# Performance work log

Hardware: AMD Instinct MI355X
Metric: run time of the kernel (lower is better)

## Reference

```python
import jax, jax.numpy as jnp
import numpy as np

BT, NQ, NC, C, H, HID = 192, 64, 1024, 384, 8, 1536
DH = C // H                       # 48
SCALE = DH ** -0.5
MAX_NEG = -float(np.finfo(np.float32).max)


def _ln(x, eps, g=None, b=None):
    m = x.mean(-1, keepdims=True)
    v = ((x - m) ** 2).mean(-1, keepdims=True)
    y = (x - m) / jnp.sqrt(v + eps)
    if g is not None:
        y = y * g + b
    return y


def _gelu_tanh(x):
    # GELU(approximate='tanh')
    return 0.5 * x * (1.0 + jnp.tanh(jnp.sqrt(2.0 / jnp.pi) * (x + 0.044715 * x ** 3)))


def setup_inputs() -> dict:
    key = jax.random.key(0)
    ks = jax.random.split(key, 10)
    s = lambda fan: 1.0 / np.sqrt(fan)
    return {
        "x": jax.random.normal(ks[0], (BT, NQ, C), jnp.float32),
        "context": jax.random.normal(ks[1], (BT, NC, C), jnp.float32),
        "mask": jax.random.randint(ks[2], (BT, NQ), 0, 2) > 0,
        "Wq": jax.random.normal(ks[3], (C, C), jnp.float32) * s(C),
        "bq": jnp.zeros((C,), jnp.float32),
        "Wkv": jax.random.normal(ks[4], (C, 2 * C), jnp.float32) * s(C),
        "bkv": jnp.zeros((2 * C,), jnp.float32),
        "Wo": jax.random.normal(ks[5], (C, C), jnp.float32) * s(C),
        "bo": jnp.zeros((C,), jnp.float32),
        "g_ctx": jnp.ones((C,), jnp.float32),
        "b_ctx": jnp.zeros((C,), jnp.float32),
        "W1": jax.random.normal(ks[6], (C, HID), jnp.float32) * s(C),
        "b1": jnp.zeros((HID,), jnp.float32),
        "W2": jax.random.normal(ks[7], (HID, C), jnp.float32) * s(HID),
        "b2": jnp.zeros((C,), jnp.float32),
    }


def reference(x, context, mask, Wq, bq, Wkv, bkv, Wo, bo, g_ctx, b_ctx, W1, b1, W2, b2):
    # --- cross-attention branch ---
    xn = _ln(x, 1e-6)                       # norm1 (no affine)
    cn = _ln(context, 1e-5, g_ctx, b_ctx)   # norm_context (affine, default eps)
    q = (xn @ Wq + bq).reshape(BT, NQ, H, DH).transpose(0, 2, 1, 3)    # (B,H,NQ,DH)
    kv = cn @ Wkv + bkv
    k, v = jnp.split(kv, 2, axis=-1)
    k = k.reshape(BT, NC, H, DH).transpose(0, 2, 1, 3)                 # (B,H,NC,DH)
    v = v.reshape(BT, NC, H, DH).transpose(0, 2, 1, 3)
    sim = jnp.einsum('bhqd,bhkd->bhqk', q, k) * SCALE                  # (B,H,NQ,NC)
    # mask shape (BT, NQ): True = keep query row; ~mask * (-max) bias
    bias = jnp.where(mask[:, None, :, None], 0.0, MAX_NEG)
    attn = jax.nn.softmax(sim + bias, axis=-1)
    o = jnp.einsum('bhqk,bhkd->bhqd', attn, v).transpose(0, 2, 1, 3).reshape(BT, NQ, C)
    x = x + o @ Wo + bo
    # --- MLP branch ---
    xn2 = _ln(x, 1e-6)                      # norm2 (no affine)
    x = x + _gelu_tanh(xn2 @ W1 + b1) @ W2 + b2
    return x
```

## Files before the change

kernel.cpp:

```cpp
#include <hip/hip_runtime.h>
#include <hip/hip_bf16.h>
#include <math.h>

typedef unsigned int  u32;
typedef unsigned short u16;
typedef unsigned char u8;

#define BTn   192
#define NQn   64
#define NCn   1024
#define Cd    384
#define Hn    8
#define DHn   48
#define HIDn  1536
#define ROWSX (BTn*NQn)
#define ROWSC (BTn*NCn)
#define ATT_SCALE 0.14433756729740643f
#define CBc   64

typedef __bf16 bf16x8 __attribute__((ext_vector_type(8)));
typedef float  f32x4  __attribute__((ext_vector_type(4)));

#define GLL16(gp, lp) __builtin_amdgcn_global_load_lds( \
    (const __attribute__((address_space(1))) void*)(gp), \
    (__attribute__((address_space(3))) void*)(lp), 16, 0, 0)

__device__ __forceinline__ float bf2f(u32 u) {
  union { u32 i; float f; } v; v.i = u << 16; return v.f;
}
__device__ __forceinline__ u16 f2bf(float f) {
  union { float f; u32 i; } v; v.f = f;
  u32 x = v.i;
  x += 0x7fffu + ((x >> 16) & 1u);
  return (u16)(x >> 16);
}
__device__ __forceinline__ void decode8(uint4 r, float* v) {
  v[0]=bf2f(r.x & 0xffffu); v[1]=bf2f(r.x >> 16);
  v[2]=bf2f(r.y & 0xffffu); v[3]=bf2f(r.y >> 16);
  v[4]=bf2f(r.z & 0xffffu); v[5]=bf2f(r.z >> 16);
  v[6]=bf2f(r.w & 0xffffu); v[7]=bf2f(r.w >> 16);
}
__device__ __forceinline__ float gelu_f(float x) {
  float x3 = x*x*x;
  float z = 0.7978845608028654f*x + 0.035677408136300125f*x3;
  float e = __expf(2.f*z);
  float th = 1.f - 2.f/(e+1.f);
  return 0.5f*x*(1.f+th);
}

__global__ void decode_mask_kernel(const u8* __restrict__ m, u8* __restrict__ keep) {
  __shared__ int flags[3];
  int t = threadIdx.x;
  if (t < 3) flags[t] = 0;
  __syncthreads();
  int nonbin = 0, oddset = 0, low01 = 0;
  for (int i = t; i < ROWSX; i += 256) {
    u32 b = m[i];
    if (b > 1u) nonbin = 1;
    if ((i & 3) && b) oddset = 1;
    if (((i & 3) < 2) && b) low01 = 1;
  }
  if (nonbin) flags[0] = 1;
  if (oddset) flags[1] = 1;
  if (low01)  flags[2] = 1;
  __syncthreads();
  int mode = flags[0] ? (flags[2] ? 2 : 3) : (flags[1] ? 1 : 0);
  for (int i = t; i < ROWSX; i += 256) {
    u8 k;
    if (mode == 2)      k = (m[2*i] | m[2*i+1]) ? 1 : 0;
    else if (mode == 3) k = (((const float*)m)[i] != 0.f) ? 1 : 0;
    else if (mode == 1) k = m[i] ? 1 : 0;
    else                k = (((const int*)m)[i] != 0) ? 1 : 0;
    keep[i] = k;
  }
}

template<int AFF, int SRCF32>
__global__ __launch_bounds__(256) void lnorm_kernel(
    const void* __restrict__ srcv, const float* __restrict__ gw,
    const float* __restrict__ bw, u16* __restrict__ dst, float eps)
{
  const int row  = blockIdx.x * 4 + (threadIdx.x >> 6);
  const int lane = threadIdx.x & 63;
  float v[6];
  if (SRCF32) {
    const float2* p = (const float2*)((const float*)srcv + (size_t)row*Cd);
    #pragma unroll
    for (int i = 0; i < 3; i++) { float2 u = p[lane + 64*i]; v[2*i]=u.x; v[2*i+1]=u.y; }
  } else {
    const u32* p = (const u32*)((const u16*)srcv + (size_t)row*Cd);
    #pragma unroll
    for (int i = 0; i < 3; i++) { u32 u = p[lane + 64*i]; v[2*i]=bf2f(u&0xffffu); v[2*i+1]=bf2f(u>>16); }
  }
  float s  = v[0]+v[1]+v[2]+v[3]+v[4]+v[5];
  float s2 = v[0]*v[0]+v[1]*v[1]+v[2]*v[2]+v[3]*v[3]+v[4]*v[4]+v[5]*v[5];
  #pragma unroll
  for (int o = 32; o >= 1; o >>= 1) { s += __shfl_xor(s, o); s2 += __shfl_xor(s2, o); }
  float mean = s * (1.0f/Cd);
  float var  = s2 * (1.0f/Cd) - mean*mean;
  var = var > 0.f ? var : 0.f;
  float rstd = rsqrtf(var + eps);
  u32* d32 = (u32*)(dst + (size_t)row*Cd);
  #pragma unroll
  for (int i = 0; i < 3; i++) {
    float y0 = (v[2*i]   - mean) * rstd;
    float y1 = (v[2*i+1] - mean) * rstd;
    if (AFF) {
      float2 gg = *(const float2*)(gw + 2*(lane + 64*i));
      float2 bb = *(const float2*)(bw + 2*(lane + 64*i));
      y0 = y0*gg.x + bb.x;
      y1 = y1*gg.y + bb.y;
    }
    d32[lane + 64*i] = (u32)f2bf(y0) | ((u32)f2bf(y1) << 16);
  }
}

__global__ __launch_bounds__(256) void wconvt_kernel(
    const float* __restrict__ W, u16* __restrict__ WT, int K, int N)
{
  __shared__ u16 tile[64][66];
  const int t  = threadIdx.x;
  const int nt = N >> 6;
  const int bk = blockIdx.x / nt, bn = blockIdx.x % nt;
  const int q  = t >> 6;
  const int nl = t & 63;
  #pragma unroll
  for (int r = 0; r < 16; r++) {
    int k = q*16 + r;
    tile[nl][k] = f2bf(W[(size_t)(bk*64 + k)*N + bn*64 + nl]);
  }
  __syncthreads();
  #pragma unroll
  for (int r = 0; r < 16; r++) {
    int n = q*16 + r;
    WT[(size_t)(bn*64 + n)*K + bk*64 + nl] = tile[n][nl];
  }
}

template<int GEL, int RES, int RF32, int OF32>
__global__ __launch_bounds__(256) void mgemm_kernel(
    const u16* __restrict__ A, const u16* __restrict__ WT,
    const float* __restrict__ bias, const void* __restrict__ resv,
    void* __restrict__ Coutv, int M, int N, int K, int nx)
{
  __shared__ u16 As[2][4096];
  __shared__ u16 Bs[2][4096];
  const int t = threadIdx.x;
  const int w = t >> 6, l = t & 63, l15 = l & 15, g = l >> 4;

  const int nwg = gridDim.x;
  const int bid = blockIdx.x;
  const int wg  = (bid & 7) * (nwg >> 3) + (bid >> 3);
  const int n0 = (wg % nx) * 128, m0 = (wg / nx) * 128;
  const int wm = (w & 1) * 64, wn = (w >> 1) * 64;

  const int arow = t >> 2;
  const int swk  = (t >> 3) & 3;
  const int acol = ((t & 3) ^ swk) * 8;
  const u16* Ag = A  + (size_t)(m0 + arow) * K + acol;
  const u16* Wg = WT + (size_t)(n0 + arow) * K + acol;
  const size_t rowskip = (size_t)64 * K;

  const int xk   = (l15 >> 1) & 3;
  const int goff = ((g ^ xk) << 3);

  f32x4 acc[4][4];
  #pragma unroll
  for (int i = 0; i < 4; i++)
    #pragma unroll
    for (int j = 0; j < 4; j++) acc[i][j] = (f32x4){0.f, 0.f, 0.f, 0.f};

#define STAGE(nb, kk) do { \
    GLL16(Ag + (kk),           &As[nb][t*8]); \
    GLL16(Ag + (kk) + rowskip, &As[nb][2048 + t*8]); \
    GLL16(Wg + (kk),           &Bs[nb][t*8]); \
    GLL16(Wg + (kk) + rowskip, &Bs[nb][2048 + t*8]); \
  } while (0)

  STAGE(0, 0);
  asm volatile("s_waitcnt vmcnt(0)" ::: "memory");
  __builtin_amdgcn_s_barrier();
  __builtin_amdgcn_sched_barrier(0);

  const int nIter = K >> 5;
  #pragma unroll 2
  for (int it = 0; it < nIter; ++it) {
    const int cur = it & 1;
    if (it + 1 < nIter) STAGE(cur ^ 1, (it + 1) << 5);
    bf16x8 af[4], bfv[4];
    #pragma unroll
    for (int i = 0; i < 4; i++)
      af[i] = *(const bf16x8*)&As[cur][(wm + i*16 + l15)*32 + goff];
    #pragma unroll
    for (int j = 0; j < 4; j++)
      bfv[j] = *(const bf16x8*)&Bs[cur][(wn + j*16 + l15)*32 + goff];
    #pragma unroll
    for (int i = 0; i < 4; i++)
      #pragma unroll
      for (int j = 0; j < 4; j++)
        acc[i][j] = __builtin_amdgcn_mfma_f32_16x16x32_bf16(bfv[j], af[i], acc[i][j], 0, 0, 0);
    asm volatile("s_waitcnt vmcnt(0)" ::: "memory");
    __builtin_amdgcn_s_barrier();
    __builtin_amdgcn_sched_barrier(0);
  }
#undef STAGE

  const float* resf = (const float*)resv;
  const u16*   resb = (const u16*)resv;
  float* Cf = (float*)Coutv;
  u16*   Cb = (u16*)Coutv;
  #pragma unroll
  for (int j = 0; j < 4; j++) {
    const int nb = n0 + wn + j*16 + g*4;
    const float4 bv = *(const float4*)&bias[nb];
    #pragma unroll
    for (int i = 0; i < 4; i++) {
      const int m = m0 + wm + i*16 + l15;
      float c0 = acc[i][j][0] + bv.x;
      float c1 = acc[i][j][1] + bv.y;
      float c2 = acc[i][j][2] + bv.z;
      float c3 = acc[i][j][3] + bv.w;
      if (GEL) { c0 = gelu_f(c0); c1 = gelu_f(c1); c2 = gelu_f(c2); c3 = gelu_f(c3); }
      if (RES) {
        if (RF32) {
          float4 r = *(const float4*)&resf[(size_t)m*N + nb];
          c0 += r.x; c1 += r.y; c2 += r.z; c3 += r.w;
        } else {
          uint2 r = *(const uint2*)&resb[(size_t)m*N + nb];
          c0 += bf2f(r.x & 0xffffu); c1 += bf2f(r.x >> 16);
          c2 += bf2f(r.y & 0xffffu); c3 += bf2f(r.y >> 16);
        }
      }
      if (OF32) {
        *(float4*)&Cf[(size_t)m*N + nb] = make_float4(c0, c1, c2, c3);
      } else {
        uint2 pk = make_uint2((u32)f2bf(c0) | ((u32)f2bf(c1) << 16),
                              (u32)f2bf(c2) | ((u32)f2bf(c3) << 16));
        *(uint2*)&Cb[(size_t)m*N + nb] = pk;
      }
    }
  }
}

__global__ __launch_bounds__(256) void fattn_kernel(
    const u16* __restrict__ qb, const u16* __restrict__ kvb,
    const u8* __restrict__ keep, u16* __restrict__ ob, int b0)
{
  __shared__ u16 Qs[64*72];
  __shared__ u16 Ks[64*72];
  __shared__ u16 Vt[48*72];
  __shared__ u16 Ps[4][16*72];

  const int t = threadIdx.x;
  const int w = t >> 6, l = t & 63, l15 = l & 15, g = l >> 4;
  const int h = blockIdx.x, bz = blockIdx.y;
  const int b = b0 + bz;
  const int wq = w * 16;

  for (int i = t; i < 2304; i += 256) { ((u32*)Qs)[i] = 0; ((u32*)Ks)[i] = 0; }
  __syncthreads();

  for (int i = t; i < 384; i += 256) {
    int row = i / 6, p = i % 6;
    uint4 v4 = *(const uint4*)(qb + (size_t)(b*NQn + row)*Cd + h*DHn + p*8);
    float f[8]; decode8(v4, f);
    u16 e[8];
    #pragma unroll
    for (int j = 0; j < 8; j++) e[j] = f2bf(f[j] * ATT_SCALE);
    uint4 pk = make_uint4((u32)e[0] | ((u32)e[1] << 16), (u32)e[2] | ((u32)e[3] << 16),
                          (u32)e[4] | ((u32)e[5] << 16), (u32)e[6] | ((u32)e[7] << 16));
    *(uint4*)&Qs[row*72 + p*8] = pk;
  }
  __syncthreads();

  bf16x8 qf0 = *(const bf16x8*)&Qs[(wq + l15)*72 + g*8];
  bf16x8 qf1 = *(const bf16x8*)&Qs[(wq + l15)*72 + 32 + g*8];

  u32 kw = *(const u32*)&keep[b*NQn + wq + g*4];
  float kf[4];
  #pragma unroll
  for (int r = 0; r < 4; r++) kf[r] = ((kw >> (8*r)) & 0xffu) ? 1.f : 0.f;

  float mrow[4], lrow[4];
  f32x4 oacc[3];
  #pragma unroll
  for (int r = 0; r < 4; r++) { mrow[r] = -3.0e38f; lrow[r] = 0.f; }
  #pragma unroll
  for (int d = 0; d < 3; d++) oacc[d] = (f32x4){0.f, 0.f, 0.f, 0.f};

  for (int kt = 0; kt < NCn/64; kt++) {
    __syncthreads();
    const size_t kbase = (size_t)bz*NCn + kt*64;
    for (int i = t; i < 384; i += 256) {
      int row = i / 6, p = i % 6;
      *(uint4*)&Ks[row*72 + p*8] =
          *(const uint4*)(kvb + (kbase + row)*(2*(size_t)Cd) + h*DHn + p*8);
    }
    if (t < 192) {
      const int dq = (t >> 4) * 4;
      const int kq = (t & 15) * 4;
      const u16* vs = kvb + (kbase + kq)*(2*(size_t)Cd) + Cd + h*DHn + dq;
      u16 q0[4], q1[4], q2[4], q3[4];
      *(uint2*)q0 = *(const uint2*)(vs);
      *(uint2*)q1 = *(const uint2*)(vs + 2*Cd);
      *(uint2*)q2 = *(const uint2*)(vs + 4*Cd);
      *(uint2*)q3 = *(const uint2*)(vs + 6*Cd);
      #pragma unroll
      for (int j = 0; j < 4; j++) {
        u16 o4[4] = {q0[j], q1[j], q2[j], q3[j]};
        *(uint2*)&Vt[(dq+j)*72 + kq] = *(uint2*)o4;
      }
    }
    __syncthreads();

    f32x4 sf[4];
    #pragma unroll
    for (int f = 0; f < 4; f++) {
      bf16x8 ka = *(const bf16x8*)&Ks[(f*16 + l15)*72 + g*8];
      bf16x8 kb = *(const bf16x8*)&Ks[(f*16 + l15)*72 + 32 + g*8];
      f32x4 z = (f32x4){0.f, 0.f, 0.f, 0.f};
      z = __builtin_amdgcn_mfma_f32_16x16x32_bf16(qf0, ka, z, 0, 0, 0);
      sf[f] = __builtin_amdgcn_mfma_f32_16x16x32_bf16(qf1, kb, z, 0, 0, 0);
    }

    float p[4][4], sc_[4];
    #pragma unroll
    for (int r = 0; r < 4; r++) {
      float pmax = fmaxf(fmaxf(sf[0][r], sf[1][r]), fmaxf(sf[2][r], sf[3][r]));
      #pragma unroll
      for (int s = 1; s < 16; s <<= 1) pmax = fmaxf(pmax, __shfl_xor(pmax, s));
      float mn = kf[r] > 0.f ? fmaxf(mrow[r], pmax) : 0.f;
      sc_[r] = kf[r] > 0.f ? __expf(mrow[r] - mn) : 1.f;
      mrow[r] = mn;
      float p0 = kf[r] > 0.f ? __expf(sf[0][r] - mn) : 1.f;
      float p1 = kf[r] > 0.f ? __expf(sf[1][r] - mn) : 1.f;
      float p2 = kf[r] > 0.f ? __expf(sf[2][r] - mn) : 1.f;
      float p3 = kf[r] > 0.f ? __expf(sf[3][r] - mn) : 1.f;
      p[0][r]=p0; p[1][r]=p1; p[2][r]=p2; p[3][r]=p3;
      float ps = p0+p1+p2+p3;
      #pragma unroll
      for (int s = 1; s < 16; s <<= 1) ps += __shfl_xor(ps, s);
      lrow[r] = lrow[r]*sc_[r] + ps;
      oacc[0][r] *= sc_[r]; oacc[1][r] *= sc_[r]; oacc[2][r] *= sc_[r];
    }

    #pragma unroll
    for (int f = 0; f < 4; f++)
      #pragma unroll
      for (int r = 0; r < 4; r++)
        Ps[w][(g*4 + r)*72 + f*16 + l15] = f2bf(p[f][r]);

    bf16x8 pa0 = *(const bf16x8*)&Ps[w][l15*72 + g*8];
    bf16x8 pa1 = *(const bf16x8*)&Ps[w][l15*72 + 32 + g*8];
    #pragma unroll
    for (int df = 0; df < 3; df++) {
      bf16x8 vb0 = *(const bf16x8*)&Vt[(df*16 + l15)*72 + g*8];
      bf16x8 vb1 = *(const bf16x8*)&Vt[(df*16 + l15)*72 + 32 + g*8];
      oacc[df] = __builtin_amdgcn_mfma_f32_16x16x32_bf16(pa0, vb0, oacc[df], 0, 0, 0);
      oacc[df] = __builtin_amdgcn_mfma_f32_16x16x32_bf16(pa1, vb1, oacc[df], 0, 0, 0);
    }
  }

  #pragma unroll
  for (int r = 0; r < 4; r++) {
    float inv = 1.f / lrow[r];
    size_t qrow = (size_t)(b*NQn + wq + g*4 + r);
    #pragma unroll
    for (int df = 0; df < 3; df++)
      ob[qrow*Cd + h*DHn + df*16 + l15] = f2bf(oacc[df][r] * inv);
  }
}

extern "C" void kernel_launch(void* const* d_in, const int* in_sizes, int n_in,
                              void* d_out, int out_size, void* d_ws, size_t ws_size,
                              hipStream_t stream) {
  (void)in_sizes; (void)n_in; (void)out_size; (void)ws_size;
  const float* x   = (const float*)d_in[0];
  const float* ctx = (const float*)d_in[1];
  const u8*    msk = (const u8*)   d_in[2];
  const float* Wq  = (const float*)d_in[3];
  const float* bq  = (const float*)d_in[4];
  const float* Wkv = (const float*)d_in[5];
  const float* bkv = (const float*)d_in[6];
  const float* Wo  = (const float*)d_in[7];
  const float* bo  = (const float*)d_in[8];
  const float* gc  = (const float*)d_in[9];
  const float* bc  = (const float*)d_in[10];
  const float* W1  = (const float*)d_in[11];
  const float* b1  = (const float*)d_in[12];
  const float* W2  = (const float*)d_in[13];
  const float* b2  = (const float*)d_in[14];
  float* out = (float*)d_out;

  char* ws = (char*)d_ws;
  size_t off = 0;
  auto bump = [&](size_t bytes) -> size_t {
    size_t o = off; off += (bytes + 255) & ~(size_t)255; return o;
  };
  const size_t act = (size_t)ROWSX * Cd * 2;
  size_t o_keep = bump(ROWSX);
  size_t o_xn   = bump(act);
  size_t o_x1n  = bump(act);
  size_t o_q    = bump(act);
  size_t o_ob   = bump(act);
  size_t o_x1   = bump(act);
  size_t o_hid  = bump((size_t)4096 * HIDn * 2);
  size_t o_wtq  = bump((size_t)Cd*Cd*2);
  size_t o_wtkv = bump((size_t)Cd*2*Cd*2);
  size_t o_wto  = bump((size_t)Cd*Cd*2);
  size_t o_wt1  = bump((size_t)Cd*HIDn*2);
  size_t o_wt2  = bump((size_t)HIDn*Cd*2);
  size_t o_cn   = bump((size_t)CBc * NCn * Cd * 2);
  size_t o_kv   = bump((size_t)CBc * NCn * 2 * Cd * 2);

  u8*  keep = (u8*)(ws + o_keep);
  u16* xn   = (u16*)(ws + o_xn);
  u16* x1n  = (u16*)(ws + o_x1n);
  u16* qb   = (u16*)(ws + o_q);
  u16* obuf = (u16*)(ws + o_ob);
  u16* x1b  = (u16*)(ws + o_x1);
  u16* hidb = (u16*)(ws + o_hid);
  u16* wtq  = (u16*)(ws + o_wtq);
  u16* wtkv = (u16*)(ws + o_wtkv);
  u16* wto  = (u16*)(ws + o_wto);
  u16* wt1  = (u16*)(ws + o_wt1);
  u16* wt2  = (u16*)(ws + o_wt2);
  u16* cnb  = (u16*)(ws + o_cn);
  u16* kvb  = (u16*)(ws + o_kv);

  decode_mask_kernel<<<1, 256, 0, stream>>>(msk, keep);

  wconvt_kernel<<<(Cd/64)*(Cd/64),     256, 0, stream>>>(Wq,  wtq,  Cd,   Cd);
  wconvt_kernel<<<(Cd/64)*(2*Cd/64),   256, 0, stream>>>(Wkv, wtkv, Cd,   2*Cd);
  wconvt_kernel<<<(Cd/64)*(Cd/64),     256, 0, stream>>>(Wo,  wto,  Cd,   Cd);
  wconvt_kernel<<<(Cd/64)*(HIDn/64),   256, 0, stream>>>(W1,  wt1,  Cd,   HIDn);
  wconvt_kernel<<<(HIDn/64)*(Cd/64),   256, 0, stream>>>(W2,  wt2,  HIDn, Cd);

  lnorm_kernel<0,1><<<ROWSX/4, 256, 0, stream>>>(x, nullptr, nullptr, xn, 1e-6f);

  mgemm_kernel<0,0,0,0><<<3*(ROWSX/128), 256, 0, stream>>>(
      xn, wtq, bq, nullptr, qb, ROWSX, Cd, Cd, 3);

  for (int b0 = 0; b0 < BTn; b0 += CBc) {
    lnorm_kernel<1,1><<<CBc*NCn/4, 256, 0, stream>>>(
        ctx + (size_t)b0*NCn*Cd, gc, bc, cnb, 1e-5f);
    mgemm_kernel<0,0,0,0><<<6*(CBc*NCn/128), 256, 0, stream>>>(
        cnb, wtkv, bkv, nullptr, kvb, CBc*NCn, 2*Cd, Cd, 6);
    fattn_kernel<<<dim3(Hn, CBc), 256, 0, stream>>>(qb, kvb, keep, obuf, b0);
  }

  mgemm_kernel<0,1,1,0><<<3*(ROWSX/128), 256, 0, stream>>>(
      obuf, wto, bo, x, x1b, ROWSX, Cd, Cd, 3);

  lnorm_kernel<0,0><<<ROWSX/4, 256, 0, stream>>>(x1b, nullptr, nullptr, x1n, 1e-6f);

  for (int rc = 0; rc < 3; rc++) {
    const size_t r0 = (size_t)rc * 4096;
    mgemm_kernel<1,0,0,0><<<12*(4096/128), 256, 0, stream>>>(
        x1n + r0*Cd, wt1, b1, nullptr, hidb, 4096, HIDn, Cd, 12);
    mgemm_kernel<0,1,0,1><<<3*(4096/128), 256, 0, stream>>>(
        hidb, wt2, b2, x1b + r0*Cd, out + r0*Cd, 4096, Cd, HIDn, 3);
  }
}
```

Baseline: 715.5 us.

## Triple-buffer GEMM K-loop and register-prefetch K/V tiles in attention

The bf16 MFMA GEMM moves from a double-buffered loop that drains all global-to-LDS loads every step to a three-stage ring. It stages two tiles ahead and waits only on the oldest group with partial vmcnt counts, so load latency overlaps more of the MFMA work. The flash-attention kernel now loads the next K/V tile from global memory into registers while the current tile is computed, then writes it to LDS, instead of loading synchronously at the top of each step. The cost is 50% more GEMM LDS, which may reduce occupancy, extra registers in attention, and barrier ordering that is harder to verify.

```diff
diff --git a/kernel.cpp b/kernel.cpp
--- a/kernel.cpp
+++ b/kernel.cpp
@@ -143,8 +143,8 @@
     const float* __restrict__ bias, const void* __restrict__ resv,
     void* __restrict__ Coutv, int M, int N, int K, int nx)
 {
-  __shared__ u16 As[2][4096];
-  __shared__ u16 Bs[2][4096];
+  __shared__ u16 As[3][4096];
+  __shared__ u16 Bs[3][4096];
   const int t = threadIdx.x;
   const int w = t >> 6, l = t & 63, l15 = l & 15, g = l >> 4;
 
@@ -170,6 +170,8 @@
     #pragma unroll
     for (int j = 0; j < 4; j++) acc[i][j] = (f32x4){0.f, 0.f, 0.f, 0.f};
 
+  const int nIter = K >> 5;
+
 #define STAGE(nb, kk) do { \
     GLL16(Ag + (kk),           &As[nb][t*8]); \
     GLL16(Ag + (kk) + rowskip, &As[nb][2048 + t*8]); \
@@ -177,32 +179,44 @@
     GLL16(Wg + (kk) + rowskip, &Bs[nb][2048 + t*8]); \
   } while (0)
 
+#define BODY(BUF, IT) do { \
+    const int it_ = (IT); \
+    if (it_ + 2 < nIter) { \
+      STAGE((BUF + 2) % 3, (it_ + 2) << 5); \
+      asm volatile("s_waitcnt vmcnt(8)" ::: "memory"); \
+    } else if (it_ + 1 < nIter) { \
+      asm volatile("s_waitcnt vmcnt(4)" ::: "memory"); \
+    } else { \
+      asm volatile("s_waitcnt vmcnt(0)" ::: "memory"); \
+    } \
+    __builtin_amdgcn_s_barrier(); \
+    __builtin_amdgcn_sched_barrier(0); \
+    { \
+      bf16x8 af[4], bfv[4]; \
+      _Pragma("unroll") \
+      for (int i = 0; i < 4; i++) \
+        af[i] = *(const bf16x8*)&As[BUF][(wm + i*16 + l15)*32 + goff]; \
+      _Pragma("unroll") \
+      for (int j = 0; j < 4; j++) \
+        bfv[j] = *(const bf16x8*)&Bs[BUF][(wn + j*16 + l15)*32 + goff]; \
+      _Pragma("unroll") \
+      for (int i = 0; i < 4; i++) \
+        _Pragma("unroll") \
+        for (int j = 0; j < 4; j++) \
+          acc[i][j] = __builtin_amdgcn_mfma_f32_16x16x32_bf16(bfv[j], af[i], acc[i][j], 0, 0, 0); \
+    } \
+    __builtin_amdgcn_sched_barrier(0); \
+    __builtin_amdgcn_s_barrier(); \
+  } while (0)
+
   STAGE(0, 0);
-  asm volatile("s_waitcnt vmcnt(0)" ::: "memory");
-  __builtin_amdgcn_s_barrier();
-  __builtin_amdgcn_sched_barrier(0);
-
-  const int nIter = K >> 5;
-  #pragma unroll 2
-  for (int it = 0; it < nIter; ++it) {
-    const int cur = it & 1;
-    if (it + 1 < nIter) STAGE(cur ^ 1, (it + 1) << 5);
-    bf16x8 af[4], bfv[4];
-    #pragma unroll
-    for (int i = 0; i < 4; i++)
-      af[i] = *(const bf16x8*)&As[cur][(wm + i*16 + l15)*32 + goff];
-    #pragma unroll
-    for (int j = 0; j < 4; j++)
-      bfv[j] = *(const bf16x8*)&Bs[cur][(wn + j*16 + l15)*32 + goff];
-    #pragma unroll
-    for (int i = 0; i < 4; i++)
-      #pragma unroll
-      for (int j = 0; j < 4; j++)
-        acc[i][j] = __builtin_amdgcn_mfma_f32_16x16x32_bf16(bfv[j], af[i], acc[i][j], 0, 0, 0);
-    asm volatile("s_waitcnt vmcnt(0)" ::: "memory");
-    __builtin_amdgcn_s_barrier();
-    __builtin_amdgcn_sched_barrier(0);
-  }
+  STAGE(1, 32);
+  for (int it0 = 0; it0 < nIter; it0 += 3) {
+    BODY(0, it0);
+    BODY(1, it0 + 1);
+    BODY(2, it0 + 2);
+  }
+#undef BODY
 #undef STAGE
 
   const float* resf = (const float*)resv;
@@ -256,6 +270,9 @@
   const int h = blockIdx.x, bz = blockIdx.y;
   const int b = b0 + bz;
   const int wq = w * 16;
+  const int krow0 = t / 6, kp0 = t % 6;
+  const int krow1 = (256 + t) / 6, kp1 = (256 + t) % 6;
+  const int vdq = (t >> 4) * 4, vkq = (t & 15) * 4;
 
   for (int i = t; i < 2304; i += 256) { ((u32*)Qs)[i] = 0; ((u32*)Ks)[i] = 0; }
   __syncthreads();
@@ -271,10 +288,6 @@
                           (u32)e[4] | ((u32)e[5] << 16), (u32)e[6] | ((u32)e[7] << 16));
     *(uint4*)&Qs[row*72 + p*8] = pk;
   }
-  __syncthreads();
-
-  bf16x8 qf0 = *(const bf16x8*)&Qs[(wq + l15)*72 + g*8];
-  bf16x8 qf1 = *(const bf16x8*)&Qs[(wq + l15)*72 + 32 + g*8];
 
   u32 kw = *(const u32*)&keep[b*NQn + wq + g*4];
   float kf[4];
@@ -288,31 +301,34 @@
   #pragma unroll
   for (int d = 0; d < 3; d++) oacc[d] = (f32x4){0.f, 0.f, 0.f, 0.f};
 
-  for (int kt = 0; kt < NCn/64; kt++) {
-    __syncthreads();
-    const size_t kbase = (size_t)bz*NCn + kt*64;
-    for (int i = t; i < 384; i += 256) {
-      int row = i / 6, p = i % 6;
-      *(uint4*)&Ks[row*72 + p*8] =
-          *(const uint4*)(kvb + (kbase + row)*(2*(size_t)Cd) + h*DHn + p*8);
-    }
+  auto loadKV = [&](int kt, uint4& KR0, uint4& KR1, uint2* V) {
+    const u16* base = kvb + ((size_t)bz*NCn + (size_t)kt*64) * (2*(size_t)Cd);
+    KR0 = *(const uint4*)(base + (size_t)krow0*(2*Cd) + h*DHn + kp0*8);
+    if (t < 128)
+      KR1 = *(const uint4*)(base + (size_t)krow1*(2*Cd) + h*DHn + kp1*8);
     if (t < 192) {
-      const int dq = (t >> 4) * 4;
-      const int kq = (t & 15) * 4;
-      const u16* vs = kvb + (kbase + kq)*(2*(size_t)Cd) + Cd + h*DHn + dq;
-      u16 q0[4], q1[4], q2[4], q3[4];
-      *(uint2*)q0 = *(const uint2*)(vs);
-      *(uint2*)q1 = *(const uint2*)(vs + 2*Cd);
-      *(uint2*)q2 = *(const uint2*)(vs + 4*Cd);
-      *(uint2*)q3 = *(const uint2*)(vs + 6*Cd);
+      const u16* vs = base + (size_t)vkq*(2*Cd) + Cd + h*DHn + vdq;
+      V[0] = *(const uint2*)(vs);
+      V[1] = *(const uint2*)(vs + 2*Cd);
+      V[2] = *(const uint2*)(vs + 4*Cd);
+      V[3] = *(const uint2*)(vs + 6*Cd);
+    }
+  };
+  auto writeKV = [&](const uint4& KR0, const uint4& KR1, const uint2* V) {
+    *(uint4*)&Ks[krow0*72 + kp0*8] = KR0;
+    if (t < 128) *(uint4*)&Ks[krow1*72 + kp1*8] = KR1;
+    if (t < 192) {
       #pragma unroll
-      for (int j = 0; j < 4; j++) {
-        u16 o4[4] = {q0[j], q1[j], q2[j], q3[j]};
-        *(uint2*)&Vt[(dq+j)*72 + kq] = *(uint2*)o4;
+      for (int jj = 0; jj < 4; jj++) {
+        u16 o4[4] = {((const u16*)&V[0])[jj], ((const u16*)&V[1])[jj],
+                     ((const u16*)&V[2])[jj], ((const u16*)&V[3])[jj]};
+        *(uint2*)&Vt[(vdq+jj)*72 + vkq] = *(uint2*)o4;
       }
     }
-    __syncthreads();
-
+  };
+
+  bf16x8 qf0, qf1;
+  auto compute = [&]() {
     f32x4 sf[4];
     #pragma unroll
     for (int f = 0; f < 4; f++) {
@@ -322,7 +338,6 @@
       z = __builtin_amdgcn_mfma_f32_16x16x32_bf16(qf0, ka, z, 0, 0, 0);
       sf[f] = __builtin_amdgcn_mfma_f32_16x16x32_bf16(qf1, kb, z, 0, 0, 0);
     }
-
     float p[4][4], sc_[4];
     #pragma unroll
     for (int r = 0; r < 4; r++) {
@@ -343,13 +358,11 @@
       lrow[r] = lrow[r]*sc_[r] + ps;
       oacc[0][r] *= sc_[r]; oacc[1][r] *= sc_[r]; oacc[2][r] *= sc_[r];
     }
-
     #pragma unroll
     for (int f = 0; f < 4; f++)
       #pragma unroll
       for (int r = 0; r < 4; r++)
         Ps[w][(g*4 + r)*72 + f*16 + l15] = f2bf(p[f][r]);
-
     bf16x8 pa0 = *(const bf16x8*)&Ps[w][l15*72 + g*8];
     bf16x8 pa1 = *(const bf16x8*)&Ps[w][l15*72 + 32 + g*8];
     #pragma unroll
@@ -358,6 +371,37 @@
       bf16x8 vb1 = *(const bf16x8*)&Vt[(df*16 + l15)*72 + 32 + g*8];
       oacc[df] = __builtin_amdgcn_mfma_f32_16x16x32_bf16(pa0, vb0, oacc[df], 0, 0, 0);
       oacc[df] = __builtin_amdgcn_mfma_f32_16x16x32_bf16(pa1, vb1, oacc[df], 0, 0, 0);
+    }
+  };
+
+  uint4 ka0, ka1, kb0_, kb1_;
+  uint2 va[4], vb_[4];
+  loadKV(0, ka0, ka1, va);
+  __syncthreads();
+
+  qf0 = *(const bf16x8*)&Qs[(wq + l15)*72 + g*8];
+  qf1 = *(const bf16x8*)&Qs[(wq + l15)*72 + 32 + g*8];
+
+  for (int kt = 0; kt < 16; kt += 2) {
+    writeKV(ka0, ka1, va);
+    asm volatile("s_waitcnt lgkmcnt(0)" ::: "memory");
+    __builtin_amdgcn_sched_barrier(0);
+    __builtin_amdgcn_s_barrier();
+    __builtin_amdgcn_sched_barrier(0);
+    loadKV(kt + 1, kb0_, kb1_, vb_);
+    compute();
+    __builtin_amdgcn_sched_barrier(0);
+    __builtin_amdgcn_s_barrier();
+    writeKV(kb0_, kb1_, vb_);
+    asm volatile("s_waitcnt lgkmcnt(0)" ::: "memory");
+    __builtin_amdgcn_sched_barrier(0);
+    __builtin_amdgcn_s_barrier();
+    __builtin_amdgcn_sched_barrier(0);
+    if (kt + 2 < 16) loadKV(kt + 2, ka0, ka1, va);
+    compute();
+    if (kt + 2 < 16) {
+      __builtin_amdgcn_sched_barrier(0);
+      __builtin_amdgcn_s_barrier();
     }
   }
 
```

After: 667.5 us. -6.7%, faster.
